# Kernel optimization log

Hardware: AMD Instinct MI355X
Metric: run time of the kernel (lower is better)

Reference implementation:

```python
import jax, jax.numpy as jnp
import numpy as np

CAPACITY_FACTOR = 1.25
NEG_INF = jnp.float32(-1e30)


def setup_inputs() -> dict:
    key = jax.random.key(0)
    k1, k2 = jax.random.split(key)
    hidden_states = jax.random.normal(k1, (4, 4096, 2048), dtype=jnp.float32)
    w_gate = jax.random.normal(k2, (64, 2048), dtype=jnp.float32) * 0.02  # nn.Linear weight [E, D]
    return {"hidden_states": hidden_states, "w_gate": w_gate}


def _switch_route(hidden_states, w_gate):
    B, S, D = hidden_states.shape
    E = w_gate.shape[0]
    N = B * S
    cap = int(N * CAPACITY_FACTOR / E)  # capacity_per_expert

    x = hidden_states.reshape(N, D)
    gate_logits = x @ w_gate.T                       # [N, E]
    gate_probs = jax.nn.softmax(gate_logits, axis=-1)
    expert_weights = jnp.max(gate_probs, axis=-1)    # [N]
    expert_indices = jnp.argmax(gate_probs, axis=-1) # [N] int

    # histogram of routed tokens per expert
    tokens_per_expert = jax.ops.segment_sum(
        jnp.ones((N,), jnp.float32), expert_indices, num_segments=E)

    cap_f = jnp.float32(cap)

    # sequential capacity-enforcement loop over experts (matches torch loop,
    # including the weight-zeroing carried across iterations)
    def step(w, e):
        mask = expert_indices == e
        masked_w = jnp.where(mask, w, NEG_INF)
        _, top_idx = jax.lax.top_k(masked_w, cap)    # top `cap` tokens of this expert
        keep = jnp.zeros((N,), bool).at[top_idx].set(True)
        w_new = w * keep.astype(w.dtype)
        w = jnp.where(tokens_per_expert[e] > cap_f, w_new, w)
        return w, None

    expert_weights, _ = jax.lax.scan(step, expert_weights, jnp.arange(E))

    mean_gate_probs = gate_probs.mean(axis=0)        # [E]
    fraction_per_expert = tokens_per_expert / N
    aux_loss = (fraction_per_expert * mean_gate_probs).sum() * E

    return expert_weights[:, None], expert_indices[:, None], tokens_per_expert, aux_loss


def reference(hidden_states, w_gate):
    return _switch_route(hidden_states, w_gate)
```

## Files before the change

### kernel.cpp

```cpp
#include <hip/hip_runtime.h>
#include <math.h>

#define DD 2048
#define EE 64
#define KQ 32
#define TOKTILE 256

__global__ __launch_bounds__(512, 4) void sr_gemm(
    const float* __restrict__ x, const float* __restrict__ wg,
    float* __restrict__ partial, int N, int ksplit)
{
  __shared__ float xs[KQ][TOKTILE];
  const int ntiles = N / TOKTILE;
  const int tt = blockIdx.x % ntiles;
  const int kc = blockIdx.x / ntiles;
  const int kblk = DD / ksplit;
  const int nchunk = kblk / KQ;
  const int k0 = kc * kblk;
  const int t0 = tt * TOKTILE;
  const int tid = threadIdx.x;
  const int ti = tid & 63;
  const int wv = __builtin_amdgcn_readfirstlane(tid >> 6);

  float acc[4][8];
#pragma unroll
  for (int r = 0; r < 4; ++r)
#pragma unroll
    for (int c = 0; c < 8; ++c) acc[r][c] = 0.f;

  const int srowbase = tid >> 3;
  const int c4 = (tid & 7) * 4;
  const int swz = 8 * (tid & 3);

  for (int ch = 0; ch < nchunk; ++ch) {
    const int kb = k0 + ch * KQ;
#pragma unroll
    for (int p = 0; p < 4; ++p) {
      const int row = p * 64 + srowbase;
      const float4 v = *reinterpret_cast<const float4*>(
          &x[(size_t)(t0 + row) * DD + kb + c4]);
      const int srow = row ^ swz;
      xs[c4 + 0][srow] = v.x;
      xs[c4 + 1][srow] = v.y;
      xs[c4 + 2][srow] = v.z;
      xs[c4 + 3][srow] = v.w;
    }
    __syncthreads();
#pragma unroll
    for (int sub = 0; sub < 8; ++sub) {
      float4 wq[8];
#pragma unroll
      for (int c = 0; c < 8; ++c)
        wq[c] = *reinterpret_cast<const float4*>(
            &wg[(size_t)(8 * wv + c) * DD + kb + 4 * sub]);
      const int sk = 8 * (sub & 3);
#pragma unroll
      for (int kk = 0; kk < 4; ++kk) {
        const int k = 4 * sub + kk;
        float xv[4];
        *reinterpret_cast<float4*>(&xv[0]) =
            *reinterpret_cast<const float4*>(&xs[k][(4 * ti) ^ sk]);
#pragma unroll
        for (int r = 0; r < 4; ++r)
#pragma unroll
          for (int c = 0; c < 8; ++c)
            acc[r][c] = fmaf(xv[r], reinterpret_cast<const float*>(&wq[c])[kk],
                             acc[r][c]);
      }
    }
    __syncthreads();
  }
#pragma unroll
  for (int c = 0; c < 8; ++c) {
    const int e = 8 * wv + c;
    const float4 v = make_float4(acc[0][c], acc[1][c], acc[2][c], acc[3][c]);
    *reinterpret_cast<float4*>(&partial[((size_t)kc * EE + e) * N + t0 + 4 * ti]) = v;
  }
}

__global__ __launch_bounds__(256) void sr_reduce(
    const float* __restrict__ partial, float* __restrict__ logits,
    int* __restrict__ counts, int N, int ksplit)
{
  if (blockIdx.x == 0 && threadIdx.x < EE) counts[threadIdx.x] = 0;
  const int i4 = blockIdx.x * 256 + threadIdx.x;
  const size_t base = (size_t)i4 * 4;
  if (base >= (size_t)EE * N) return;
  const size_t cs = (size_t)EE * N;
  double s0 = 0.0, s1 = 0.0, s2 = 0.0, s3 = 0.0;
  for (int c = 0; c < ksplit; ++c) {
    const float4 v = *reinterpret_cast<const float4*>(&partial[c * cs + base]);
    s0 += (double)v.x; s1 += (double)v.y; s2 += (double)v.z; s3 += (double)v.w;
  }
  *reinterpret_cast<float4*>(&logits[base]) =
      make_float4((float)s0, (float)s1, (float)s2, (float)s3);
}

__global__ __launch_bounds__(256) void sr_softmax(
    const float* __restrict__ logits, float* __restrict__ dout,
    float* __restrict__ ws_w, int* __restrict__ ws_idx,
    int* __restrict__ counts, float* __restrict__ probsum, int N)
{
  __shared__ float lp[128][EE + 1];
  __shared__ float psq[4][EE];
  const int tid = threadIdx.x;
  const int t0 = blockIdx.x * 128;
  if (tid < 128) {
    const int t = t0 + tid;
    float l[EE];
    float maxv = -3.0e38f;
    int arg = 0;
#pragma unroll
    for (int e = 0; e < EE; ++e) {
      l[e] = logits[(size_t)e * N + t];
      if (l[e] > maxv) { maxv = l[e]; arg = e; }
    }
    float s = 0.f;
#pragma unroll
    for (int e = 0; e < EE; ++e) {
      const float ex = __expf(l[e] - maxv);
      lp[tid][e] = ex;
      s += ex;
    }
    const float inv = 1.0f / s;
    const float w = inv;
#pragma unroll
    for (int e = 0; e < EE; ++e) lp[tid][e] *= inv;
    dout[t] = w;
    dout[N + t] = (float)arg;
    ws_w[t] = w;
    ws_idx[t] = arg;
    atomicAdd(&counts[arg], 1);
  }
  __syncthreads();
  const int e = tid & 63, q = tid >> 6;
  float ps = 0.f;
  for (int r = 0; r < 32; ++r) ps += lp[q * 32 + r][e];
  psq[q][e] = ps;
  __syncthreads();
  if (tid < 64) {
    const float tot = ((psq[0][tid] + psq[1][tid]) + psq[2][tid]) + psq[3][tid];
    probsum[(size_t)blockIdx.x * EE + tid] = tot;
  }
}

__global__ __launch_bounds__(256) void sr_stats(
    const float* __restrict__ probsum, const int* __restrict__ counts,
    float* __restrict__ dout, int* __restrict__ header,
    int N, int nblocks, int cap)
{
  __shared__ double dq[4][EE];
  __shared__ double mean_s[EE];
  __shared__ int cnt_s[EE];
  const int tid = threadIdx.x;
  const int e = tid & 63, q = tid >> 6;
  const int per = nblocks / 4;
  double ps = 0.0;
  for (int b = q * per; b < (q + 1) * per; ++b)
    ps += (double)probsum[(size_t)b * EE + e];
  dq[q][e] = ps;
  __syncthreads();
  if (tid < 64) {
    const double tot = ((dq[0][tid] + dq[1][tid]) + dq[2][tid]) + dq[3][tid];
    const int cnt = counts[tid];
    dout[2 * N + tid] = (float)cnt;
    mean_s[tid] = tot / (double)N;
    cnt_s[tid] = cnt;
  }
  __syncthreads();
  if (tid == 0) {
    double aux = 0.0;
    int nover = 0, e1 = -1;
    for (int i = 0; i < EE; ++i) {
      aux += ((double)cnt_s[i] / (double)N) * mean_s[i];
      if (cnt_s[i] > cap) { if (nover == 0) e1 = i; ++nover; }
    }
    dout[2 * N + EE] = (float)(aux * (double)EE);
    header[0] = (nover >= 2) ? 2 : nover;
    header[1] = e1;
  }
}

__device__ __forceinline__ int sr_bsum(int c, int red[][16], int pc, int tid) {
#pragma unroll
  for (int off = 32; off > 0; off >>= 1) c += __shfl_down(c, off, 64);
  if ((tid & 63) == 0) red[pc & 1][tid >> 6] = c;
  __syncthreads();
  int s = 0;
#pragma unroll
  for (int i = 0; i < 16; ++i) s += red[pc & 1][i];
  return s;
}

__global__ __launch_bounds__(1024) void sr_select(
    const float* __restrict__ ws_w, const int* __restrict__ ws_idx,
    int* __restrict__ header, int N, int cap)
{
  __shared__ int red[2][16];
  const int tid = threadIdx.x;
  const int mode = header[0];
  if (mode != 1) {
    if (tid == 0) { header[2] = 0; header[3] = N; }
    return;
  }
  const int e1 = header[1];
  unsigned mb[16];
  const int PER = N / 1024;
  for (int r = 0; r < 16; ++r) {
    unsigned b = 0u;
    if (r < PER) {
      const int i = tid + r * 1024;
      if (ws_idx[i] == e1) b = __float_as_uint(ws_w[i]);
    }
    mb[r] = b;
  }
  int pc = 0;
  unsigned lo = 0x3C000000u, hi = 0x3F800000u;
  while (hi - lo > 1u) {
    const unsigned mid = lo + ((hi - lo) >> 1);
    int c = 0;
#pragma unroll
    for (int r = 0; r < 16; ++r) c += (mb[r] >= mid);
    const int tot = sr_bsum(c, red, pc++, tid);
    if (tot >= cap) lo = mid; else hi = mid;
  }
  int cge = 0, cgt = 0;
#pragma unroll
  for (int r = 0; r < 16; ++r) {
    cge += (mb[r] >= lo);
    cgt += (mb[r] > lo);
  }
  const int tot_ge = sr_bsum(cge, red, pc++, tid);
  const int tot_gt = sr_bsum(cgt, red, pc++, tid);
  const int quota = cap - tot_gt;
  int idx_thr = N - 1;
  if (tot_ge - tot_gt > quota) {
    int l2 = -1, h2 = N - 1;
    while (h2 - l2 > 1) {
      const int mid = (l2 + h2) >> 1;
      int c = 0;
#pragma unroll
      for (int r = 0; r < 16; ++r) {
        const int i = tid + r * 1024;
        c += (mb[r] == lo && mb[r] != 0u && i <= mid) ? 1 : 0;
      }
      const int tot = sr_bsum(c, red, pc++, tid);
      if (tot >= quota) h2 = mid; else l2 = mid;
    }
    idx_thr = h2;
  }
  if (tid == 0) { header[2] = (int)lo; header[3] = idx_thr; }
}

__global__ __launch_bounds__(256) void sr_apply(
    const float* __restrict__ ws_w, const int* __restrict__ ws_idx,
    const int* __restrict__ header, float* __restrict__ dout, int N)
{
  const int i = blockIdx.x * 256 + threadIdx.x;
  if (i >= N) return;
  const int mode = header[0];
  const float w = ws_w[i];
  float out = w;
  if (mode == 2) {
    out = 0.f;
  } else if (mode == 1) {
    const int e1 = header[1];
    const unsigned tau = (unsigned)header[2];
    const int ithr = header[3];
    const unsigned b = __float_as_uint(w);
    const bool keep = (ws_idx[i] == e1) && (b > tau || (b == tau && i <= ithr));
    out = keep ? w : 0.f;
  }
  dout[i] = out;
}

extern "C" void kernel_launch(void* const* d_in, const int* in_sizes, int n_in,
                              void* d_out, int out_size, void* d_ws, size_t ws_size,
                              hipStream_t stream)
{
  const float* x = (const float*)d_in[0];
  const float* wg = (const float*)d_in[1];
  const int N = in_sizes[0] / DD;
  float* dout = (float*)d_out;
  float* wsf = (float*)d_ws;

  float* ws_w = wsf;
  int* ws_idx = (int*)(wsf + N);
  int* counts = (int*)(wsf + 2 * (size_t)N);
  float* probsum = wsf + 2 * (size_t)N + EE;
  const int nblocks_sm = N / 128;
  int* header = (int*)(wsf + 2 * (size_t)N + EE + (size_t)nblocks_sm * EE);
  float* logits = wsf + 2 * (size_t)N + EE + (size_t)nblocks_sm * EE + 16;
  float* partial = logits + (size_t)EE * N;
  const size_t base_floats = 2 * (size_t)N + EE + (size_t)nblocks_sm * EE + 16 + (size_t)EE * N;

  int ksplit = 8;
  while (ksplit > 1 &&
         (base_floats + (size_t)ksplit * EE * (size_t)N) * sizeof(float) > ws_size)
    ksplit >>= 1;
  const int cap = (int)((double)N * 1.25 / (double)EE);

  sr_gemm<<<(N / TOKTILE) * ksplit, 512, 0, stream>>>(x, wg, partial, N, ksplit);
  sr_reduce<<<(EE * N / 4 + 255) / 256, 256, 0, stream>>>(partial, logits, counts, N, ksplit);
  sr_softmax<<<N / 128, 256, 0, stream>>>(logits, dout, ws_w, ws_idx, counts, probsum, N);
  sr_stats<<<1, 256, 0, stream>>>(probsum, counts, dout, header, N, nblocks_sm, cap);
  sr_select<<<1, 1024, 0, stream>>>(ws_w, ws_idx, header, N, cap);
  sr_apply<<<(N + 255) / 256, 256, 0, stream>>>(ws_w, ws_idx, header, dout, N);
}
```

Measured before the change: 156.2 us.

## Enlarge GEMM register tile, stage gate weights in LDS, prefetch next chunk

The gate GEMM now uses 256 threads each computing a 16x8 register tile over a 512-token tile. The gate weight chunk is staged in shared memory instead of being read per wave from global memory, and the next x/w chunk is prefetched into registers while the current one is computed. The ksplit is fixed at 8, dropping the workspace-size fallback. The aim is more FMAs per LDS load and hidden global-load latency. The cost is much higher register pressure (128 accumulators plus 64 prefetch registers) and fewer blocks, 256 instead of 512, which lowers occupancy.

```diff
diff --git a/kernel.cpp b/kernel.cpp
--- a/kernel.cpp
+++ b/kernel.cpp
@@ -4,77 +4,103 @@
 #define DD 2048
 #define EE 64
 #define KQ 32
-#define TOKTILE 256
-
-__global__ __launch_bounds__(512, 4) void sr_gemm(
+#define TOKTILE 512
+#define KSPLIT 8
+
+__global__ __launch_bounds__(256, 1) void sr_gemm(
     const float* __restrict__ x, const float* __restrict__ wg,
-    float* __restrict__ partial, int N, int ksplit)
+    float* __restrict__ partial, int N)
 {
   __shared__ float xs[KQ][TOKTILE];
+  __shared__ float wsh[KQ][EE];
   const int ntiles = N / TOKTILE;
   const int tt = blockIdx.x % ntiles;
   const int kc = blockIdx.x / ntiles;
-  const int kblk = DD / ksplit;
+  const int kblk = DD / KSPLIT;
   const int nchunk = kblk / KQ;
   const int k0 = kc * kblk;
   const int t0 = tt * TOKTILE;
   const int tid = threadIdx.x;
-  const int ti = tid & 63;
-  const int wv = __builtin_amdgcn_readfirstlane(tid >> 6);
-
-  float acc[4][8];
-#pragma unroll
-  for (int r = 0; r < 4; ++r)
+  const int tq = tid >> 3;
+  const int te = tid & 7;
+  const int lrow = tid >> 3;
+  const int lc4 = (tid & 7) * 4;
+  const int lswz = 16 * (tid & 3);
+  const int we = tid >> 2;
+  const int wkq = (tid & 3) * 8;
+
+  float acc[16][8];
+#pragma unroll
+  for (int r = 0; r < 16; ++r)
 #pragma unroll
     for (int c = 0; c < 8; ++c) acc[r][c] = 0.f;
 
-  const int srowbase = tid >> 3;
-  const int c4 = (tid & 7) * 4;
-  const int swz = 8 * (tid & 3);
+  float4 vx[16];
+  float4 vw0, vw1;
+
+#pragma unroll
+  for (int p = 0; p < 16; ++p)
+    vx[p] = *reinterpret_cast<const float4*>(
+        &x[(size_t)(t0 + p * 32 + lrow) * DD + k0 + lc4]);
+  vw0 = *reinterpret_cast<const float4*>(&wg[(size_t)we * DD + k0 + wkq]);
+  vw1 = *reinterpret_cast<const float4*>(&wg[(size_t)we * DD + k0 + wkq + 4]);
 
   for (int ch = 0; ch < nchunk; ++ch) {
-    const int kb = k0 + ch * KQ;
-#pragma unroll
-    for (int p = 0; p < 4; ++p) {
-      const int row = p * 64 + srowbase;
-      const float4 v = *reinterpret_cast<const float4*>(
-          &x[(size_t)(t0 + row) * DD + kb + c4]);
-      const int srow = row ^ swz;
-      xs[c4 + 0][srow] = v.x;
-      xs[c4 + 1][srow] = v.y;
-      xs[c4 + 2][srow] = v.z;
-      xs[c4 + 3][srow] = v.w;
-    }
     __syncthreads();
 #pragma unroll
-    for (int sub = 0; sub < 8; ++sub) {
-      float4 wq[8];
-#pragma unroll
-      for (int c = 0; c < 8; ++c)
-        wq[c] = *reinterpret_cast<const float4*>(
-            &wg[(size_t)(8 * wv + c) * DD + kb + 4 * sub]);
-      const int sk = 8 * (sub & 3);
-#pragma unroll
-      for (int kk = 0; kk < 4; ++kk) {
-        const int k = 4 * sub + kk;
-        float xv[4];
-        *reinterpret_cast<float4*>(&xv[0]) =
-            *reinterpret_cast<const float4*>(&xs[k][(4 * ti) ^ sk]);
-#pragma unroll
-        for (int r = 0; r < 4; ++r)
-#pragma unroll
-          for (int c = 0; c < 8; ++c)
-            acc[r][c] = fmaf(xv[r], reinterpret_cast<const float*>(&wq[c])[kk],
-                             acc[r][c]);
-      }
-    }
+    for (int p = 0; p < 16; ++p) {
+      const int srow = (p * 32 + lrow) ^ lswz;
+      xs[lc4 + 0][srow] = vx[p].x;
+      xs[lc4 + 1][srow] = vx[p].y;
+      xs[lc4 + 2][srow] = vx[p].z;
+      xs[lc4 + 3][srow] = vx[p].w;
+    }
+    wsh[wkq + 0][we] = vw0.x; wsh[wkq + 1][we] = vw0.y;
+    wsh[wkq + 2][we] = vw0.z; wsh[wkq + 3][we] = vw0.w;
+    wsh[wkq + 4][we] = vw1.x; wsh[wkq + 5][we] = vw1.y;
+    wsh[wkq + 6][we] = vw1.z; wsh[wkq + 7][we] = vw1.w;
     __syncthreads();
+    if (ch + 1 < nchunk) {
+      const int kb = k0 + (ch + 1) * KQ;
+#pragma unroll
+      for (int p = 0; p < 16; ++p)
+        vx[p] = *reinterpret_cast<const float4*>(
+            &x[(size_t)(t0 + p * 32 + lrow) * DD + kb + lc4]);
+      vw0 = *reinterpret_cast<const float4*>(&wg[(size_t)we * DD + kb + wkq]);
+      vw1 = *reinterpret_cast<const float4*>(&wg[(size_t)we * DD + kb + wkq + 4]);
+    }
+#pragma unroll
+    for (int k = 0; k < KQ; ++k) {
+      const int sk = 16 * ((k >> 2) & 3);
+      float xv[16], wv[8];
+      *reinterpret_cast<float4*>(&xv[0]) =
+          *reinterpret_cast<const float4*>(&xs[k][(4 * tq + 0) ^ sk]);
+      *reinterpret_cast<float4*>(&xv[4]) =
+          *reinterpret_cast<const float4*>(&xs[k][(4 * tq + 128) ^ sk]);
+      *reinterpret_cast<float4*>(&xv[8]) =
+          *reinterpret_cast<const float4*>(&xs[k][(4 * tq + 256) ^ sk]);
+      *reinterpret_cast<float4*>(&xv[12]) =
+          *reinterpret_cast<const float4*>(&xs[k][(4 * tq + 384) ^ sk]);
+      *reinterpret_cast<float4*>(&wv[0]) =
+          *reinterpret_cast<const float4*>(&wsh[k][8 * te]);
+      *reinterpret_cast<float4*>(&wv[4]) =
+          *reinterpret_cast<const float4*>(&wsh[k][8 * te + 4]);
+#pragma unroll
+      for (int r = 0; r < 16; ++r)
+#pragma unroll
+        for (int c = 0; c < 8; ++c) acc[r][c] = fmaf(xv[r], wv[c], acc[r][c]);
+    }
   }
 #pragma unroll
   for (int c = 0; c < 8; ++c) {
-    const int e = 8 * wv + c;
-    const float4 v = make_float4(acc[0][c], acc[1][c], acc[2][c], acc[3][c]);
-    *reinterpret_cast<float4*>(&partial[((size_t)kc * EE + e) * N + t0 + 4 * ti]) = v;
+    const int e = 8 * te + c;
+#pragma unroll
+    for (int g = 0; g < 4; ++g) {
+      const float4 v = make_float4(acc[4 * g + 0][c], acc[4 * g + 1][c],
+                                   acc[4 * g + 2][c], acc[4 * g + 3][c]);
+      *reinterpret_cast<float4*>(
+          &partial[((size_t)kc * EE + e) * N + t0 + 4 * tq + 128 * g]) = v;
+    }
   }
 }
 
@@ -292,16 +318,10 @@
   int* header = (int*)(wsf + 2 * (size_t)N + EE + (size_t)nblocks_sm * EE);
   float* logits = wsf + 2 * (size_t)N + EE + (size_t)nblocks_sm * EE + 16;
   float* partial = logits + (size_t)EE * N;
-  const size_t base_floats = 2 * (size_t)N + EE + (size_t)nblocks_sm * EE + 16 + (size_t)EE * N;
-
-  int ksplit = 8;
-  while (ksplit > 1 &&
-         (base_floats + (size_t)ksplit * EE * (size_t)N) * sizeof(float) > ws_size)
-    ksplit >>= 1;
   const int cap = (int)((double)N * 1.25 / (double)EE);
 
-  sr_gemm<<<(N / TOKTILE) * ksplit, 512, 0, stream>>>(x, wg, partial, N, ksplit);
-  sr_reduce<<<(EE * N / 4 + 255) / 256, 256, 0, stream>>>(partial, logits, counts, N, ksplit);
+  sr_gemm<<<(N / TOKTILE) * KSPLIT, 256, 0, stream>>>(x, wg, partial, N);
+  sr_reduce<<<(EE * N / 4 + 255) / 256, 256, 0, stream>>>(partial, logits, counts, N, KSPLIT);
   sr_softmax<<<N / 128, 256, 0, stream>>>(logits, dout, ws_w, ws_idx, counts, probsum, N);
   sr_stats<<<1, 256, 0, stream>>>(probsum, counts, dout, header, N, nblocks_sm, cap);
   sr_select<<<1, 1024, 0, stream>>>(ws_w, ws_idx, header, N, cap);
```

Measured after the change: 161.0 us. 3.0% more time.

## Stage gate weights in shared memory and halve GEMM token tile

Applied to the files above, without the earlier changes.

Each GEMM block now loads its K-chunk of the 64-expert gate weights into a shared-memory tile, instead of every wavefront reading float4 weight rows directly from global memory. The token tile shrinks from 256 to 128 and the block from 512 to 256 threads. Each thread now covers 4 tokens by 8 experts indexed by lane groups of 32, so one wave reads weights for two expert groups. This removes redundant global and L1 weight traffic and doubles the block count, at the cost of an extra shared-memory write and read per k and some bank conflicts on the transposed store.

```diff
diff --git a/kernel.cpp b/kernel.cpp
--- a/kernel.cpp
+++ b/kernel.cpp
@@ -4,13 +4,14 @@
 #define DD 2048
 #define EE 64
 #define KQ 32
-#define TOKTILE 256
-
-__global__ __launch_bounds__(512, 4) void sr_gemm(
+#define TOKTILE 128
+
+__global__ __launch_bounds__(256, 4) void sr_gemm(
     const float* __restrict__ x, const float* __restrict__ wg,
     float* __restrict__ partial, int N, int ksplit)
 {
   __shared__ float xs[KQ][TOKTILE];
+  __shared__ float wsh[KQ][EE];
   const int ntiles = N / TOKTILE;
   const int tt = blockIdx.x % ntiles;
   const int kc = blockIdx.x / ntiles;
@@ -19,8 +20,8 @@
   const int k0 = kc * kblk;
   const int t0 = tt * TOKTILE;
   const int tid = threadIdx.x;
-  const int ti = tid & 63;
-  const int wv = __builtin_amdgcn_readfirstlane(tid >> 6);
+  const int ti = tid & 31;
+  const int tj = tid >> 5;
 
   float acc[4][8];
 #pragma unroll
@@ -36,7 +37,7 @@
     const int kb = k0 + ch * KQ;
 #pragma unroll
     for (int p = 0; p < 4; ++p) {
-      const int row = p * 64 + srowbase;
+      const int row = p * 32 + srowbase;
       const float4 v = *reinterpret_cast<const float4*>(
           &x[(size_t)(t0 + row) * DD + kb + c4]);
       const int srow = row ^ swz;
@@ -45,34 +46,33 @@
       xs[c4 + 2][srow] = v.z;
       xs[c4 + 3][srow] = v.w;
     }
+    {
+      const int e = tid >> 2;
+      const int kq = (tid & 3) * 8;
+      const float4 a = *reinterpret_cast<const float4*>(&wg[(size_t)e * DD + kb + kq]);
+      const float4 b = *reinterpret_cast<const float4*>(&wg[(size_t)e * DD + kb + kq + 4]);
+      wsh[kq + 0][e] = a.x; wsh[kq + 1][e] = a.y; wsh[kq + 2][e] = a.z; wsh[kq + 3][e] = a.w;
+      wsh[kq + 4][e] = b.x; wsh[kq + 5][e] = b.y; wsh[kq + 6][e] = b.z; wsh[kq + 7][e] = b.w;
+    }
     __syncthreads();
-#pragma unroll
-    for (int sub = 0; sub < 8; ++sub) {
-      float4 wq[8];
-#pragma unroll
-      for (int c = 0; c < 8; ++c)
-        wq[c] = *reinterpret_cast<const float4*>(
-            &wg[(size_t)(8 * wv + c) * DD + kb + 4 * sub]);
-      const int sk = 8 * (sub & 3);
-#pragma unroll
-      for (int kk = 0; kk < 4; ++kk) {
-        const int k = 4 * sub + kk;
-        float xv[4];
-        *reinterpret_cast<float4*>(&xv[0]) =
-            *reinterpret_cast<const float4*>(&xs[k][(4 * ti) ^ sk]);
-#pragma unroll
-        for (int r = 0; r < 4; ++r)
-#pragma unroll
-          for (int c = 0; c < 8; ++c)
-            acc[r][c] = fmaf(xv[r], reinterpret_cast<const float*>(&wq[c])[kk],
-                             acc[r][c]);
-      }
+#pragma unroll 8
+    for (int k = 0; k < KQ; ++k) {
+      const int sk = 8 * ((k >> 2) & 3);
+      float xv[4], wv[8];
+      *reinterpret_cast<float4*>(&xv[0]) =
+          *reinterpret_cast<const float4*>(&xs[k][(4 * ti) ^ sk]);
+      *reinterpret_cast<float4*>(&wv[0]) = *reinterpret_cast<const float4*>(&wsh[k][8 * tj]);
+      *reinterpret_cast<float4*>(&wv[4]) = *reinterpret_cast<const float4*>(&wsh[k][8 * tj + 4]);
+#pragma unroll
+      for (int r = 0; r < 4; ++r)
+#pragma unroll
+        for (int c = 0; c < 8; ++c) acc[r][c] = fmaf(xv[r], wv[c], acc[r][c]);
     }
     __syncthreads();
   }
 #pragma unroll
   for (int c = 0; c < 8; ++c) {
-    const int e = 8 * wv + c;
+    const int e = 8 * tj + c;
     const float4 v = make_float4(acc[0][c], acc[1][c], acc[2][c], acc[3][c]);
     *reinterpret_cast<float4*>(&partial[((size_t)kc * EE + e) * N + t0 + 4 * ti]) = v;
   }
@@ -300,7 +300,7 @@
     ksplit >>= 1;
   const int cap = (int)((double)N * 1.25 / (double)EE);
 
-  sr_gemm<<<(N / TOKTILE) * ksplit, 512, 0, stream>>>(x, wg, partial, N, ksplit);
+  sr_gemm<<<(N / TOKTILE) * ksplit, 256, 0, stream>>>(x, wg, partial, N, ksplit);
   sr_reduce<<<(EE * N / 4 + 255) / 256, 256, 0, stream>>>(partial, logits, counts, N, ksplit);
   sr_softmax<<<N / 128, 256, 0, stream>>>(logits, dout, ws_w, ws_idx, counts, probsum, N);
   sr_stats<<<1, 256, 0, stream>>>(probsum, counts, dout, header, N, nblocks_sm, cap);
```

Result: faster. 144.6 us (-7.5%).

## Halve GEMM token tile and fuse stats, select and apply into one kernel

Applied to the files above, without the earlier changes.

Shrinks the gate GEMM tile to 128 tokens with 256 threads, doubling the number of blocks, and maps expert groups to half-waves. Merges the stats, capacity-selection and apply kernels into a single 1024-thread block that keeps weights and indices in registers. This removes two launches and the global header round-trip. The cost is less weight reuse per block, non-uniform weight loads within a wave, and a single block writing the final weights.

```diff
diff --git a/kernel.cpp b/kernel.cpp
--- a/kernel.cpp
+++ b/kernel.cpp
@@ -4,9 +4,9 @@
 #define DD 2048
 #define EE 64
 #define KQ 32
-#define TOKTILE 256
-
-__global__ __launch_bounds__(512, 4) void sr_gemm(
+#define TOKTILE 128
+
+__global__ __launch_bounds__(256, 4) void sr_gemm(
     const float* __restrict__ x, const float* __restrict__ wg,
     float* __restrict__ partial, int N, int ksplit)
 {
@@ -19,8 +19,8 @@
   const int k0 = kc * kblk;
   const int t0 = tt * TOKTILE;
   const int tid = threadIdx.x;
-  const int ti = tid & 63;
-  const int wv = __builtin_amdgcn_readfirstlane(tid >> 6);
+  const int ti = tid & 31;
+  const int tj = tid >> 5;
 
   float acc[4][8];
 #pragma unroll
@@ -36,7 +36,7 @@
     const int kb = k0 + ch * KQ;
 #pragma unroll
     for (int p = 0; p < 4; ++p) {
-      const int row = p * 64 + srowbase;
+      const int row = p * 32 + srowbase;
       const float4 v = *reinterpret_cast<const float4*>(
           &x[(size_t)(t0 + row) * DD + kb + c4]);
       const int srow = row ^ swz;
@@ -52,7 +52,7 @@
 #pragma unroll
       for (int c = 0; c < 8; ++c)
         wq[c] = *reinterpret_cast<const float4*>(
-            &wg[(size_t)(8 * wv + c) * DD + kb + 4 * sub]);
+            &wg[(size_t)(8 * tj + c) * DD + kb + 4 * sub]);
       const int sk = 8 * (sub & 3);
 #pragma unroll
       for (int kk = 0; kk < 4; ++kk) {
@@ -72,7 +72,7 @@
   }
 #pragma unroll
   for (int c = 0; c < 8; ++c) {
-    const int e = 8 * wv + c;
+    const int e = 8 * tj + c;
     const float4 v = make_float4(acc[0][c], acc[1][c], acc[2][c], acc[3][c]);
     *reinterpret_cast<float4*>(&partial[((size_t)kc * EE + e) * N + t0 + 4 * ti]) = v;
   }
@@ -144,24 +144,56 @@
   }
 }
 
-__global__ __launch_bounds__(256) void sr_stats(
+__device__ __forceinline__ int sr_bsum(int c, int red[][16], int pc, int tid) {
+#pragma unroll
+  for (int off = 32; off > 0; off >>= 1) c += __shfl_down(c, off, 64);
+  if ((tid & 63) == 0) red[pc & 1][tid >> 6] = c;
+  __syncthreads();
+  int s = 0;
+#pragma unroll
+  for (int i = 0; i < 16; ++i) s += red[pc & 1][i];
+  return s;
+}
+
+__global__ __launch_bounds__(1024) void sr_finish(
     const float* __restrict__ probsum, const int* __restrict__ counts,
-    float* __restrict__ dout, int* __restrict__ header,
-    int N, int nblocks, int cap)
-{
-  __shared__ double dq[4][EE];
+    const float* __restrict__ ws_w, const int* __restrict__ ws_idx,
+    float* __restrict__ dout, int N, int nblocks, int cap)
+{
+  __shared__ double dseg[16][EE];
   __shared__ double mean_s[EE];
   __shared__ int cnt_s[EE];
+  __shared__ int hdr[2];
+  __shared__ int red[2][16];
   const int tid = threadIdx.x;
-  const int e = tid & 63, q = tid >> 6;
-  const int per = nblocks / 4;
-  double ps = 0.0;
-  for (int b = q * per; b < (q + 1) * per; ++b)
-    ps += (double)probsum[(size_t)b * EE + e];
-  dq[q][e] = ps;
+  const int PER = N / 1024;
+
+  float wv[16];
+  int iv[16];
+#pragma unroll
+  for (int r = 0; r < 16; ++r) {
+    float w = 0.f; int ix = -1;
+    if (r < PER) {
+      const int i = tid + r * 1024;
+      w = ws_w[i];
+      ix = ws_idx[i];
+    }
+    wv[r] = w; iv[r] = ix;
+  }
+
+  {
+    const int e = tid & 63, seg = tid >> 6;
+    const int per = nblocks / 16;
+    double ps = 0.0;
+    for (int b = seg * per; b < (seg + 1) * per; ++b)
+      ps += (double)probsum[(size_t)b * EE + e];
+    dseg[seg][e] = ps;
+  }
   __syncthreads();
   if (tid < 64) {
-    const double tot = ((dq[0][tid] + dq[1][tid]) + dq[2][tid]) + dq[3][tid];
+    double tot = 0.0;
+#pragma unroll
+    for (int s2 = 0; s2 < 16; ++s2) tot += dseg[s2][tid];
     const int cnt = counts[tid];
     dout[2 * N + tid] = (float)cnt;
     mean_s[tid] = tot / (double)N;
@@ -176,44 +208,26 @@
       if (cnt_s[i] > cap) { if (nover == 0) e1 = i; ++nover; }
     }
     dout[2 * N + EE] = (float)(aux * (double)EE);
-    header[0] = (nover >= 2) ? 2 : nover;
-    header[1] = e1;
-  }
-}
-
-__device__ __forceinline__ int sr_bsum(int c, int red[][16], int pc, int tid) {
-#pragma unroll
-  for (int off = 32; off > 0; off >>= 1) c += __shfl_down(c, off, 64);
-  if ((tid & 63) == 0) red[pc & 1][tid >> 6] = c;
-  __syncthreads();
-  int s = 0;
-#pragma unroll
-  for (int i = 0; i < 16; ++i) s += red[pc & 1][i];
-  return s;
-}
-
-__global__ __launch_bounds__(1024) void sr_select(
-    const float* __restrict__ ws_w, const int* __restrict__ ws_idx,
-    int* __restrict__ header, int N, int cap)
-{
-  __shared__ int red[2][16];
-  const int tid = threadIdx.x;
-  const int mode = header[0];
-  if (mode != 1) {
-    if (tid == 0) { header[2] = 0; header[3] = N; }
+    hdr[0] = (nover >= 2) ? 2 : nover;
+    hdr[1] = e1;
+  }
+  __syncthreads();
+  const int mode = hdr[0];
+
+  if (mode == 0) return;
+  if (mode == 2) {
+#pragma unroll
+    for (int r = 0; r < 16; ++r)
+      if (r < PER) dout[tid + r * 1024] = 0.f;
     return;
   }
-  const int e1 = header[1];
+
+  const int e1 = hdr[1];
   unsigned mb[16];
-  const int PER = N / 1024;
-  for (int r = 0; r < 16; ++r) {
-    unsigned b = 0u;
-    if (r < PER) {
-      const int i = tid + r * 1024;
-      if (ws_idx[i] == e1) b = __float_as_uint(ws_w[i]);
-    }
-    mb[r] = b;
-  }
+#pragma unroll
+  for (int r = 0; r < 16; ++r)
+    mb[r] = (iv[r] == e1) ? __float_as_uint(wv[r]) : 0u;
+
   int pc = 0;
   unsigned lo = 0x3C000000u, hi = 0x3F800000u;
   while (hi - lo > 1u) {
@@ -242,36 +256,22 @@
 #pragma unroll
       for (int r = 0; r < 16; ++r) {
         const int i = tid + r * 1024;
-        c += (mb[r] == lo && mb[r] != 0u && i <= mid) ? 1 : 0;
+        c += (mb[r] == lo && i <= mid) ? 1 : 0;
       }
       const int tot = sr_bsum(c, red, pc++, tid);
       if (tot >= quota) h2 = mid; else l2 = mid;
     }
     idx_thr = h2;
   }
-  if (tid == 0) { header[2] = (int)lo; header[3] = idx_thr; }
-}
-
-__global__ __launch_bounds__(256) void sr_apply(
-    const float* __restrict__ ws_w, const int* __restrict__ ws_idx,
-    const int* __restrict__ header, float* __restrict__ dout, int N)
-{
-  const int i = blockIdx.x * 256 + threadIdx.x;
-  if (i >= N) return;
-  const int mode = header[0];
-  const float w = ws_w[i];
-  float out = w;
-  if (mode == 2) {
-    out = 0.f;
-  } else if (mode == 1) {
-    const int e1 = header[1];
-    const unsigned tau = (unsigned)header[2];
-    const int ithr = header[3];
-    const unsigned b = __float_as_uint(w);
-    const bool keep = (ws_idx[i] == e1) && (b > tau || (b == tau && i <= ithr));
-    out = keep ? w : 0.f;
-  }
-  dout[i] = out;
+
+#pragma unroll
+  for (int r = 0; r < 16; ++r) {
+    if (r < PER) {
+      const int i = tid + r * 1024;
+      const bool keep = (mb[r] > lo) || (mb[r] == lo && i <= idx_thr);
+      dout[i] = keep ? wv[r] : 0.f;
+    }
+  }
 }
 
 extern "C" void kernel_launch(void* const* d_in, const int* in_sizes, int n_in,
@@ -289,10 +289,9 @@
   int* counts = (int*)(wsf + 2 * (size_t)N);
   float* probsum = wsf + 2 * (size_t)N + EE;
   const int nblocks_sm = N / 128;
-  int* header = (int*)(wsf + 2 * (size_t)N + EE + (size_t)nblocks_sm * EE);
-  float* logits = wsf + 2 * (size_t)N + EE + (size_t)nblocks_sm * EE + 16;
+  float* logits = wsf + 2 * (size_t)N + EE + (size_t)nblocks_sm * EE;
   float* partial = logits + (size_t)EE * N;
-  const size_t base_floats = 2 * (size_t)N + EE + (size_t)nblocks_sm * EE + 16 + (size_t)EE * N;
+  const size_t base_floats = 2 * (size_t)N + EE + (size_t)nblocks_sm * EE + (size_t)EE * N;
 
   int ksplit = 8;
   while (ksplit > 1 &&
@@ -300,10 +299,8 @@
     ksplit >>= 1;
   const int cap = (int)((double)N * 1.25 / (double)EE);
 
-  sr_gemm<<<(N / TOKTILE) * ksplit, 512, 0, stream>>>(x, wg, partial, N, ksplit);
+  sr_gemm<<<(N / TOKTILE) * ksplit, 256, 0, stream>>>(x, wg, partial, N, ksplit);
   sr_reduce<<<(EE * N / 4 + 255) / 256, 256, 0, stream>>>(partial, logits, counts, N, ksplit);
   sr_softmax<<<N / 128, 256, 0, stream>>>(logits, dout, ws_w, ws_idx, counts, probsum, N);
-  sr_stats<<<1, 256, 0, stream>>>(probsum, counts, dout, header, N, nblocks_sm, cap);
-  sr_select<<<1, 1024, 0, stream>>>(ws_w, ws_idx, header, N, cap);
-  sr_apply<<<(N + 255) / 256, 256, 0, stream>>>(ws_w, ws_idx, header, dout, N);
-}
+  sr_finish<<<1, 1024, 0, stream>>>(probsum, counts, ws_w, ws_idx, dout, N, nblocks_sm, cap);
+}
```

Measured after the change: 145.5 us. 1.07x faster.
